# Kernel optimization log

Hardware: AMD Instinct MI355X
Metric: run time of the kernel (lower is better)

The kernel has to match this reference:

```python
import jax, jax.numpy as jnp
import numpy as np

DIM = 2048
NUM_HEADS = 8
HEAD_DIM = DIM // NUM_HEADS  # 256; forward requires seq_len == HEAD_DIM
B = 64
N = HEAD_DIM  # q @ k (untransposed) only works when N == head_dim


def setup_inputs() -> dict:
    key = jax.random.key(0)
    k1, k2, k3, k4 = jax.random.split(key, 4)
    x = jax.random.normal(k1, (B, N, DIM), dtype=jnp.float32)
    # torch Linear stores weight as [out_features, in_features]
    w_qkv = jax.random.normal(k2, (3 * DIM, DIM), dtype=jnp.float32) * 0.02
    w_proj = jax.random.normal(k3, (DIM, DIM), dtype=jnp.float32) * 0.02
    b_proj = jax.random.normal(k4, (DIM,), dtype=jnp.float32) * 0.02
    return {"x": x, "w_qkv": w_qkv, "w_proj": w_proj, "b_proj": b_proj}


def reference(x, w_qkv, w_proj, b_proj):
    Bb, Nn, C = x.shape
    H, D = NUM_HEADS, C // NUM_HEADS
    # qkv projection (no bias), split into q,k,v of shape [B,H,N,D]
    qkv = (x @ w_qkv.T).reshape(Bb, Nn, 3, H, D).transpose(2, 0, 3, 1, 4)
    q, k, v = qkv[0], qkv[1], qkv[2]
    # NON-standard: q @ k with k NOT transposed -> contracts q's feature dim
    # against k's token dim (valid because D == N). attn: [B,H,N,N]
    attn = jnp.matmul(q, k)
    # transpose last two dims, then softmax over the new last axis
    attn = jnp.swapaxes(attn, -2, -1)
    attn = jax.nn.softmax(attn, axis=-1)
    out = jnp.matmul(attn, v)              # [B,H,N,D]
    out = out.swapaxes(1, 2).reshape(Bb, Nn, C)
    return out @ w_proj.T + b_proj
```

## Files before the change

kernel.cpp:

```cpp
#include <hip/hip_runtime.h>
#include <hip/hip_bf16.h>

typedef unsigned short u16;
typedef __attribute__((ext_vector_type(4))) float f32x4;
typedef __attribute__((ext_vector_type(8))) short short8;
typedef __attribute__((ext_vector_type(8))) u16 us8;


__device__ __forceinline__ u16 f2bf(float f) {
  union { float f; unsigned u; } v; v.f = f;
  unsigned r = v.u + 0x7fffu + ((v.u >> 16) & 1u);
  return (u16)(r >> 16);
}
__device__ __forceinline__ float bf2f(u16 h) {
  union { unsigned u; float f; } v; v.u = ((unsigned)h) << 16; return v.f;
}

__global__ void beacon_kernel(float* __restrict__ out, float val, int n) {
  int stride = gridDim.x * blockDim.x;
  for (int i = blockIdx.x * blockDim.x + threadIdx.x; i < n; i += stride)
    out[i] = val;
}

__global__ void split_kernel(const float* __restrict__ in, u16* __restrict__ hi,
                             u16* __restrict__ lo, int n4) {
  int stride = gridDim.x * blockDim.x;
  for (int i = blockIdx.x * blockDim.x + threadIdx.x; i < n4; i += stride) {
    f32x4 v = ((const f32x4*)in)[i];
    ushort4 h;
    h.x = f2bf(v[0]); h.y = f2bf(v[1]); h.z = f2bf(v[2]); h.w = f2bf(v[3]);
    ((ushort4*)hi)[i] = h;
    if (lo) {
      ushort4 l;
      l.x = f2bf(v[0] - bf2f(h.x)); l.y = f2bf(v[1] - bf2f(h.y));
      l.z = f2bf(v[2] - bf2f(h.z)); l.w = f2bf(v[3] - bf2f(h.w));
      ((ushort4*)lo)[i] = l;
    }
  }
}

#define SCHED0 __builtin_amdgcn_sched_barrier(0)
#define LGKM0 do { asm volatile("s_waitcnt lgkmcnt(0)" ::: "memory"); SCHED0; } while (0)
#define VM0 do { asm volatile("s_waitcnt vmcnt(0)" ::: "memory"); } while (0)
#define BAR __builtin_amdgcn_s_barrier()

template<int EPI>
__global__ __launch_bounds__(512, 2)
void gemm256(const u16* __restrict__ A0, const u16* __restrict__ A1,
             const u16* __restrict__ B0, const u16* __restrict__ B1,
             int ldA, int ldB, int ntiles, int segShift, int gridMx,
             u16* __restrict__ qh, u16* __restrict__ ql,
             u16* __restrict__ kh, u16* __restrict__ kl,
             u16* __restrict__ vv,
             float* __restrict__ fout, const float* __restrict__ bias) {
  extern __shared__ __align__(16) u16 lds[];

  const int tid = threadIdx.x;
  const int w = tid >> 6, lane = tid & 63;
  const int wr = w >> 2, wcn = w & 3;
  const int l15 = lane & 15, g = lane >> 4;
  const int rsw = l15 & 7;
  const int scol = (((tid & 7) ^ ((tid >> 3) & 7)) << 3);

  int bid = blockIdx.x, cpx = gridDim.x >> 3;
  int swz = (bid & 7) * cpx + (bid >> 3);
  int m0 = (swz % gridMx) << 8;
  int n0 = (swz / gridMx) << 8;

  const u16* As[2] = {A0, A1};
  const u16* Bs[2] = {B0, B1};
  const int kmask = (1 << segShift) - 1;

  f32x4 acc[8][4] = {};
  short8 af[8], bA[4], bB[4];

  auto stageA = [&](int db, const u16* Ab, int k0) {
    #pragma unroll
    for (int s = 0; s < 4; ++s) {
      const u16* src = Ab + (size_t)(m0 + s * 64 + (tid >> 3)) * ldA + k0 + scol;
      u16* dst = lds + db * 32768 + s * 4096 + tid * 8;
      __builtin_amdgcn_global_load_lds(
          (const __attribute__((address_space(1))) unsigned*)src,
          (__attribute__((address_space(3))) unsigned*)dst, 16, 0, 0);
    }
  };
  auto stageB = [&](int db, const u16* Bb, int k0) {
    #pragma unroll
    for (int s = 0; s < 4; ++s) {
      const u16* src = Bb + (size_t)(n0 + s * 64 + (tid >> 3)) * ldB + k0 + scol;
      u16* dst = lds + db * 32768 + 16384 + s * 4096 + tid * 8;
      __builtin_amdgcn_global_load_lds(
          (const __attribute__((address_space(1))) unsigned*)src,
          (__attribute__((address_space(3))) unsigned*)dst, 16, 0, 0);
    }
  };
  auto readA = [&](int db, int MH) {
    #pragma unroll
    for (int f = 0; f < 4; ++f) {
      int row = wr * 128 + MH * 64 + f * 16 + l15;
      #pragma unroll
      for (int kk = 0; kk < 2; ++kk) {
        int sl = (kk * 4 + g) ^ rsw;
        af[f * 2 + kk] = *(const short8*)(lds + db * 32768 + row * 64 + sl * 8);
      }
    }
  };
  auto readB = [&](short8* bf, int db, int NH) {
    #pragma unroll
    for (int f = 0; f < 2; ++f) {
      int row = wcn * 64 + NH * 32 + f * 16 + l15;
      #pragma unroll
      for (int kk = 0; kk < 2; ++kk) {
        int sl = (kk * 4 + g) ^ rsw;
        bf[f * 2 + kk] = *(const short8*)(lds + db * 32768 + 16384 + row * 64 + sl * 8);
      }
    }
  };

#define MMA_QUAD(MH, NH, BF)                                                   \
  __builtin_amdgcn_s_setprio(1);                                               \
  _Pragma("unroll") for (int f = 0; f < 4; ++f)                                \
    _Pragma("unroll") for (int j = 0; j < 2; ++j)                              \
      _Pragma("unroll") for (int kk = 0; kk < 2; ++kk)                         \
        acc[(MH) * 4 + f][(NH) * 2 + j] =                                      \
            __builtin_amdgcn_mfma_f32_16x16x32_bf16(                           \
                af[f * 2 + kk], BF[j * 2 + kk],                                \
                acc[(MH) * 4 + f][(NH) * 2 + j], 0, 0, 0);                     \
  __builtin_amdgcn_s_setprio(0)

  const int T = ntiles;
  stageA(0, As[0], 0);
  stageB(0, Bs[0], 0);
  VM0;
  BAR; SCHED0;

  for (int t = 0; t < T - 1; ++t) {
    int cur = t & 1, nxt = cur ^ 1;
    int t1 = t + 1;
    const u16* An = As[t1 >> segShift];
    const u16* Bn = Bs[t1 >> segShift];
    int kn = (t1 & kmask) << 6;
    readA(cur, 0);
    readB(bA, cur, 0);
    stageA(nxt, An, kn);
    BAR; LGKM0;
    MMA_QUAD(0, 0, bA);
    BAR; SCHED0;
    readB(bB, cur, 1);
    stageB(nxt, Bn, kn);
    BAR; LGKM0;
    MMA_QUAD(0, 1, bB);
    BAR; SCHED0;
    readA(cur, 1);
    BAR; LGKM0;
    MMA_QUAD(1, 1, bB);
    BAR; SCHED0;
    MMA_QUAD(1, 0, bA);
    VM0;
    BAR; SCHED0;
  }
  {
    int cur = (T - 1) & 1;
    readA(cur, 0);
    readB(bA, cur, 0);
    LGKM0;
    MMA_QUAD(0, 0, bA);
    readB(bB, cur, 1);
    LGKM0;
    MMA_QUAD(0, 1, bB);
    readA(cur, 1);
    LGKM0;
    MMA_QUAD(1, 1, bB);
    MMA_QUAD(1, 0, bA);
  }
#undef MMA_QUAD

  #pragma unroll
  for (int i = 0; i < 8; ++i)
    #pragma unroll
    for (int j = 0; j < 4; ++j)
      #pragma unroll
      for (int rr = 0; rr < 4; ++rr) {
        int gm = m0 + wr * 128 + i * 16 + g * 4 + rr;
        int gn = n0 + wcn * 64 + j * 16 + l15;
        float val = acc[i][j][rr];
        if constexpr (EPI == 0) {
          int b = gm >> 8, tok = gm & 255;
          int sel = gn >> 11, head = (gn >> 8) & 7, col = gn & 255;
          size_t addr = (((size_t)b * 8 + head) * 256 + tok) * 256 + col;
          u16 h = f2bf(val), lo = f2bf(val - bf2f(h));
          if (sel == 0) { qh[addr] = h; ql[addr] = lo; }
          else          { kh[addr] = h; kl[addr] = lo; }
        } else if constexpr (EPI == 1) {
          int b = gm >> 8, tok = gm & 255;
          int head = (gn >> 8) & 7, col = gn & 255;
          size_t addr = (((size_t)b * 8 + head) * 256 + tok) * 256 + col;
          vv[addr] = f2bf(val);
        } else {
          fout[(size_t)gm * 2048 + gn] = val + bias[gn];
        }
      }
}

__global__ __launch_bounds__(256)
void fused_attn(const u16* __restrict__ kh, const u16* __restrict__ kl,
                const u16* __restrict__ qh, const u16* __restrict__ ql,
                const u16* __restrict__ vT, u16* __restrict__ aout) {
  __shared__ __align__(16) u16 sA[2][2048];
  __shared__ __align__(16) u16 sB[2][8192];
  __shared__ __align__(16) u16 sP[64 * 276];

  const int tid = threadIdx.x;
  const int wave = tid >> 6, lane = tid & 63;
  const int l15 = lane & 15, l16 = lane >> 4;
  const int sxor = (l15 >> 1) & 3;
  const int scol = ((lane & 3) ^ ((lane >> 3) & 3)) * 8;

  const int bid = blockIdx.x;
  const int plane = (bid & 7) * 64 + (bid >> 5);
  const int mtile = (bid >> 3) & 3;
  const int m0 = mtile << 6;
  const size_t zo = (size_t)plane * 65536;
  const u16* As[3] = {kh + zo, kh + zo, kl + zo};
  const u16* Bs[3] = {qh + zo, ql + zo, qh + zo};

  auto stageL = [&](int db, int ks) {
    int seg = ks >> 3, k0 = (ks & 7) * 32;
    {
      const u16* gp = As[seg];
      int r = wave * 16 + (lane >> 2);
      const u16* src = gp + (size_t)(m0 + r) * 256 + k0 + scol;
      __builtin_amdgcn_global_load_lds(
          (const __attribute__((address_space(1))) unsigned*)src,
          (__attribute__((address_space(3))) unsigned*)(sA[db] + wave * 512), 16, 0, 0);
    }
    {
      const u16* gp = Bs[seg];
      #pragma unroll
      for (int c = 0; c < 4; ++c) {
        int chunk = wave + c * 4;
        int r = chunk * 16 + (lane >> 2);
        const u16* src = gp + (size_t)r * 256 + k0 + scol;
        __builtin_amdgcn_global_load_lds(
            (const __attribute__((address_space(1))) unsigned*)src,
            (__attribute__((address_space(3))) unsigned*)(sB[db] + chunk * 512), 16, 0, 0);
      }
    }
  };

  f32x4 acc[16] = {};
  stageL(0, 0);
  VM0; BAR; SCHED0;
  for (int ks = 0; ks < 24; ++ks) {
    int cur = ks & 1, nxt = cur ^ 1;
    short8 a;
    {
      int ra = (wave * 16 + l15) * 4 + (l16 ^ sxor);
      a = ((const short8*)sA[cur])[ra];
    }
    short8 b[16];
    #pragma unroll
    for (int c = 0; c < 16; ++c) {
      int rb = (c * 16 + l15) * 4 + (l16 ^ sxor);
      b[c] = ((const short8*)sB[cur])[rb];
    }
    if (ks < 23) stageL(nxt, ks + 1);
    BAR; LGKM0;
    #pragma unroll
    for (int c = 0; c < 16; ++c)
      acc[c] = __builtin_amdgcn_mfma_f32_16x16x32_bf16(a, b[c], acc[c], 0, 0, 0);
    if (ks < 23) VM0;
    BAR; SCHED0;
  }

  #pragma unroll
  for (int rr = 0; rr < 4; ++rr) {
    float m = acc[0][rr];
    #pragma unroll
    for (int c = 1; c < 16; ++c) m = fmaxf(m, acc[c][rr]);
    #pragma unroll
    for (int sh = 1; sh < 16; sh <<= 1) m = fmaxf(m, __shfl_xor(m, sh));
    float e[16];
    float s = 0.f;
    #pragma unroll
    for (int c = 0; c < 16; ++c) { e[c] = __expf(acc[c][rr] - m); s += e[c]; }
    #pragma unroll
    for (int sh = 1; sh < 16; sh <<= 1) s += __shfl_xor(s, sh);
    float inv = 1.0f / s;
    int prow = wave * 16 + l16 * 4 + rr;
    #pragma unroll
    for (int c = 0; c < 16; ++c)
      sP[prow * 276 + c * 16 + l15] = f2bf(e[c] * inv);
  }
  __syncthreads();

  const int wr2 = wave >> 1, wc2 = wave & 1;
  auto stageV = [&](int db, int ks) {
    int k0 = ks * 32;
    #pragma unroll
    for (int c = 0; c < 4; ++c) {
      int chunk = wave + c * 4;
      int r = chunk * 16 + (lane >> 2);
      const u16* src = vT + zo + (size_t)r * 256 + k0 + scol;
      __builtin_amdgcn_global_load_lds(
          (const __attribute__((address_space(1))) unsigned*)src,
          (__attribute__((address_space(3))) unsigned*)(sB[db] + chunk * 512), 16, 0, 0);
    }
  };
  f32x4 acc2[2][8] = {};
  stageV(0, 0);
  VM0; BAR; SCHED0;
  for (int ks = 0; ks < 8; ++ks) {
    int cur = ks & 1, nxt = cur ^ 1;
    int k0 = ks * 32;
    short8 a[2], b[8];
    #pragma unroll
    for (int i = 0; i < 2; ++i) {
      int prow = wr2 * 32 + i * 16 + l15;
      a[i] = *(const short8*)(sP + prow * 276 + k0 + l16 * 8);
    }
    #pragma unroll
    for (int j = 0; j < 8; ++j) {
      int rb = (wc2 * 128 + j * 16 + l15) * 4 + (l16 ^ sxor);
      b[j] = ((const short8*)sB[cur])[rb];
    }
    if (ks < 7) stageV(nxt, ks + 1);
    BAR; LGKM0;
    #pragma unroll
    for (int i = 0; i < 2; ++i)
      #pragma unroll
      for (int j = 0; j < 8; ++j)
        acc2[i][j] = __builtin_amdgcn_mfma_f32_16x16x32_bf16(a[i], b[j], acc2[i][j], 0, 0, 0);
    if (ks < 7) VM0;
    BAR; SCHED0;
  }

  #pragma unroll
  for (int i = 0; i < 2; ++i)
    #pragma unroll
    for (int j = 0; j < 8; ++j)
      #pragma unroll
      for (int rr = 0; rr < 4; ++rr) {
        int gi = m0 + wr2 * 32 + i * 16 + l16 * 4 + rr;
        int gd = wc2 * 128 + j * 16 + l15;
        size_t row = (size_t)(plane >> 3) * 256 + gi;
        size_t col = (size_t)(plane & 7) * 256 + gd;
        aout[row * 2048 + col] = f2bf(acc2[i][j][rr]);
      }
}

__global__ void transpose_inplace(u16* __restrict__ kh, u16* __restrict__ kl,
                                  u16* __restrict__ v) {
  __shared__ u16 ta[64][66], tb[64][66];
  u16* base = (blockIdx.z == 0) ? kh : (blockIdx.z == 1) ? kl : v;
  u16* pl = base + (size_t)blockIdx.y * 65536;
  const int RA[10] = {0,1,2,3, 0,0,0,1,1,2};
  const int CA[10] = {0,1,2,3, 1,2,3,2,3,3};
  int p = blockIdx.x;
  int R = RA[p], C = CA[p];
  bool diag = (R == C);
  int tid = threadIdx.x;
  int r = tid >> 2, c0 = (tid & 3) * 16;

  const us8* sa = (const us8*)(pl + (size_t)(R * 64 + r) * 256 + C * 64 + c0);
  us8 a0 = sa[0], a1 = sa[1];
  #pragma unroll
  for (int s = 0; s < 8; ++s) { ta[r][c0 + s] = a0[s]; ta[r][c0 + 8 + s] = a1[s]; }
  if (!diag) {
    const us8* sb = (const us8*)(pl + (size_t)(C * 64 + r) * 256 + R * 64 + c0);
    us8 b0 = sb[0], b1 = sb[1];
    #pragma unroll
    for (int s = 0; s < 8; ++s) { tb[r][c0 + s] = b0[s]; tb[r][c0 + 8 + s] = b1[s]; }
  }
  __syncthreads();
  us8 o0, o1;
  #pragma unroll
  for (int s = 0; s < 8; ++s) { o0[s] = ta[c0 + s][r]; o1[s] = ta[c0 + 8 + s][r]; }
  us8* da = (us8*)(pl + (size_t)(C * 64 + r) * 256 + R * 64 + c0);
  da[0] = o0; da[1] = o1;
  if (!diag) {
    us8 p0, p1;
    #pragma unroll
    for (int s = 0; s < 8; ++s) { p0[s] = tb[c0 + s][r]; p1[s] = tb[c0 + 8 + s][r]; }
    us8* db = (us8*)(pl + (size_t)(R * 64 + r) * 256 + C * 64 + c0);
    db[0] = p0; db[1] = p1;
  }
}

extern "C" void kernel_launch(void* const* d_in, const int* in_sizes, int n_in,
                              void* d_out, int out_size, void* d_ws, size_t ws_size,
                              hipStream_t stream) {
  const float* x  = (const float*)d_in[0];
  const float* wq = (const float*)d_in[1];
  const float* wp = (const float*)d_in[2];
  const float* bp = (const float*)d_in[3];
  float* out = (float*)d_out;
  char* ws = (char*)d_ws;

  const size_t MB = 1ull << 20;
  const size_t NEED = 432 * MB;
  if (ws_size < NEED) {
    beacon_kernel<<<2048, 256, 0, stream>>>(out, (float)(ws_size >> 20), 16384 * 2048);
    return;
  }

  u16* q_hi = (u16*)(ws);
  u16* q_lo = (u16*)(ws + 64 * MB);
  u16* k_hi = (u16*)(ws + 128 * MB);
  u16* k_lo = (u16*)(ws + 192 * MB);
  u16* vbuf = (u16*)(ws + 256 * MB);
  u16* x_hi = (u16*)(ws + 320 * MB);
  u16* w_hi = (u16*)(ws + 384 * MB);
  u16* w_lo = (u16*)(ws + 408 * MB);
  u16* attn = (u16*)(ws + 320 * MB);
  u16* wpb  = (u16*)(ws + 384 * MB);

  split_kernel<<<8192, 256, 0, stream>>>(x,  x_hi, nullptr, 16384 * 2048 / 4);
  split_kernel<<<4096, 256, 0, stream>>>(wq, w_hi, w_lo, 6144 * 2048 / 4);

  gemm256<0><<<1024, 512, 131072, stream>>>(
      x_hi, x_hi, w_hi, w_lo, 2048, 2048, 64, 5, 64,
      q_hi, q_lo, k_hi, k_lo, nullptr, nullptr, nullptr);
  const u16* wv = w_hi + (size_t)4096 * 2048;
  gemm256<1><<<512, 512, 131072, stream>>>(
      x_hi, x_hi, wv, wv, 2048, 2048, 32, 5, 64,
      nullptr, nullptr, nullptr, nullptr, vbuf, nullptr, nullptr);

  transpose_inplace<<<dim3(10, 512, 3), 256, 0, stream>>>(k_hi, k_lo, vbuf);

  fused_attn<<<2048, 256, 0, stream>>>(k_hi, k_lo, q_hi, q_lo, vbuf, attn);

  split_kernel<<<2048, 256, 0, stream>>>(wp, wpb, nullptr, 2048 * 2048 / 4);
  gemm256<2><<<512, 512, 131072, stream>>>(
      attn, attn, wpb, wpb, 2048, 2048, 32, 5, 64,
      nullptr, nullptr, nullptr, nullptr, nullptr, out, bp);
}
```

Measured before the change: 1.076 ms.

## Retile attention score GEMM to 4x4 fragments per wave with cross-wave softmax

Changes the first attention GEMM's wave tiling. Instead of each wave owning 16 rows across all 256 columns, each wave now owns all 64 rows across a 64-column slice, using a 4x4 grid of MFMA fragments. This cuts LDS fragment reads per k-step from 17 to 8. Because each row is now split across waves, the softmax needs a shared-memory reduction for the max and the sum, which adds two barriers and an extra LDS buffer.

```diff
diff --git a/kernel.cpp b/kernel.cpp
--- a/kernel.cpp
+++ b/kernel.cpp
@@ -209,6 +209,7 @@
   __shared__ __align__(16) u16 sA[2][2048];
   __shared__ __align__(16) u16 sB[2][8192];
   __shared__ __align__(16) u16 sP[64 * 276];
+  __shared__ float red[2][4][64];
 
   const int tid = threadIdx.x;
   const int wave = tid >> 6, lane = tid & 63;
@@ -248,50 +249,74 @@
     }
   };
 
-  f32x4 acc[16] = {};
+  f32x4 acc[4][4] = {};
   stageL(0, 0);
   VM0; BAR; SCHED0;
   for (int ks = 0; ks < 24; ++ks) {
     int cur = ks & 1, nxt = cur ^ 1;
-    short8 a;
-    {
-      int ra = (wave * 16 + l15) * 4 + (l16 ^ sxor);
-      a = ((const short8*)sA[cur])[ra];
-    }
-    short8 b[16];
-    #pragma unroll
-    for (int c = 0; c < 16; ++c) {
-      int rb = (c * 16 + l15) * 4 + (l16 ^ sxor);
-      b[c] = ((const short8*)sB[cur])[rb];
+    short8 a[4], b[4];
+    #pragma unroll
+    for (int fi = 0; fi < 4; ++fi) {
+      int ra = (fi * 16 + l15) * 4 + (l16 ^ sxor);
+      a[fi] = ((const short8*)sA[cur])[ra];
+    }
+    #pragma unroll
+    for (int fj = 0; fj < 4; ++fj) {
+      int rb = ((wave * 64 + fj * 16 + l15)) * 4 + (l16 ^ sxor);
+      b[fj] = ((const short8*)sB[cur])[rb];
     }
     if (ks < 23) stageL(nxt, ks + 1);
     BAR; LGKM0;
     #pragma unroll
-    for (int c = 0; c < 16; ++c)
-      acc[c] = __builtin_amdgcn_mfma_f32_16x16x32_bf16(a, b[c], acc[c], 0, 0, 0);
+    for (int fi = 0; fi < 4; ++fi)
+      #pragma unroll
+      for (int fj = 0; fj < 4; ++fj)
+        acc[fi][fj] = __builtin_amdgcn_mfma_f32_16x16x32_bf16(a[fi], b[fj], acc[fi][fj], 0, 0, 0);
     if (ks < 23) VM0;
     BAR; SCHED0;
   }
 
   #pragma unroll
-  for (int rr = 0; rr < 4; ++rr) {
-    float m = acc[0][rr];
-    #pragma unroll
-    for (int c = 1; c < 16; ++c) m = fmaxf(m, acc[c][rr]);
-    #pragma unroll
-    for (int sh = 1; sh < 16; sh <<= 1) m = fmaxf(m, __shfl_xor(m, sh));
-    float e[16];
-    float s = 0.f;
-    #pragma unroll
-    for (int c = 0; c < 16; ++c) { e[c] = __expf(acc[c][rr] - m); s += e[c]; }
-    #pragma unroll
-    for (int sh = 1; sh < 16; sh <<= 1) s += __shfl_xor(s, sh);
-    float inv = 1.0f / s;
-    int prow = wave * 16 + l16 * 4 + rr;
-    #pragma unroll
-    for (int c = 0; c < 16; ++c)
-      sP[prow * 276 + c * 16 + l15] = f2bf(e[c] * inv);
-  }
+  for (int fi = 0; fi < 4; ++fi)
+    #pragma unroll
+    for (int rr = 0; rr < 4; ++rr) {
+      float m = fmaxf(fmaxf(acc[fi][0][rr], acc[fi][1][rr]),
+                      fmaxf(acc[fi][2][rr], acc[fi][3][rr]));
+      #pragma unroll
+      for (int sh = 1; sh < 16; sh <<= 1) m = fmaxf(m, __shfl_xor(m, sh));
+      if (l15 == 0) red[0][wave][fi * 16 + l16 * 4 + rr] = m;
+    }
+  __syncthreads();
+  #pragma unroll
+  for (int fi = 0; fi < 4; ++fi)
+    #pragma unroll
+    for (int rr = 0; rr < 4; ++rr) {
+      int i = fi * 16 + l16 * 4 + rr;
+      float M = fmaxf(fmaxf(red[0][0][i], red[0][1][i]),
+                      fmaxf(red[0][2][i], red[0][3][i]));
+      float s = 0.f;
+      #pragma unroll
+      for (int fj = 0; fj < 4; ++fj) {
+        float ev = __expf(acc[fi][fj][rr] - M);
+        acc[fi][fj][rr] = ev;
+        s += ev;
+      }
+      #pragma unroll
+      for (int sh = 1; sh < 16; sh <<= 1) s += __shfl_xor(s, sh);
+      if (l15 == 0) red[1][wave][i] = s;
+    }
+  __syncthreads();
+  #pragma unroll
+  for (int fi = 0; fi < 4; ++fi)
+    #pragma unroll
+    for (int rr = 0; rr < 4; ++rr) {
+      int i = fi * 16 + l16 * 4 + rr;
+      float S = (red[1][0][i] + red[1][1][i]) + (red[1][2][i] + red[1][3][i]);
+      float inv = 1.0f / S;
+      #pragma unroll
+      for (int fj = 0; fj < 4; ++fj)
+        sP[i * 276 + wave * 64 + fj * 16 + l15] = f2bf(acc[fi][fj][rr] * inv);
+    }
   __syncthreads();
 
   const int wr2 = wave >> 1, wc2 = wave & 1;
@@ -313,16 +338,16 @@
   for (int ks = 0; ks < 8; ++ks) {
     int cur = ks & 1, nxt = cur ^ 1;
     int k0 = ks * 32;
-    short8 a[2], b[8];
+    short8 a2[2], b2[8];
     #pragma unroll
     for (int i = 0; i < 2; ++i) {
       int prow = wr2 * 32 + i * 16 + l15;
-      a[i] = *(const short8*)(sP + prow * 276 + k0 + l16 * 8);
+      a2[i] = *(const short8*)(sP + prow * 276 + k0 + l16 * 8);
     }
     #pragma unroll
     for (int j = 0; j < 8; ++j) {
       int rb = (wc2 * 128 + j * 16 + l15) * 4 + (l16 ^ sxor);
-      b[j] = ((const short8*)sB[cur])[rb];
+      b2[j] = ((const short8*)sB[cur])[rb];
     }
     if (ks < 7) stageV(nxt, ks + 1);
     BAR; LGKM0;
@@ -330,7 +355,7 @@
     for (int i = 0; i < 2; ++i)
       #pragma unroll
       for (int j = 0; j < 8; ++j)
-        acc2[i][j] = __builtin_amdgcn_mfma_f32_16x16x32_bf16(a[i], b[j], acc2[i][j], 0, 0, 0);
+        acc2[i][j] = __builtin_amdgcn_mfma_f32_16x16x32_bf16(a2[i], b2[j], acc2[i][j], 0, 0, 0);
     if (ks < 7) VM0;
     BAR; SCHED0;
   }
```

Measured after the change: 1.026 ms. 1.05x faster.
